# Performance work log

Measured on AMD Instinct MI355X. Metric: run time of the kernel, lower is better.

## Reference

```python
import jax, jax.numpy as jnp
import numpy as np

LEAK_RATE = 0.2
SPECTRAL_RADIUS = 0.9


def setup_inputs() -> dict:
    key = jax.random.key(0)
    k1, k2, k3 = jax.random.split(key, 3)
    B, T, D, U = 32, 1024, 256, 1024
    # glorot-uniform-like init
    lim_w = np.sqrt(6.0 / (U + U)).astype(np.float32)
    lim_in = np.sqrt(6.0 / (D + U)).astype(np.float32)
    W = jax.random.uniform(k1, (U, U), jnp.float32, -lim_w, lim_w)
    # rescale reservoir to target spectral radius (done once at build, like the tf layer)
    eig = np.linalg.eigvals(np.asarray(W))
    W = W * (SPECTRAL_RADIUS / np.max(np.abs(eig)).astype(np.float32))
    W_in = jax.random.uniform(k2, (D, U), jnp.float32, -lim_in, lim_in)
    x = jax.random.normal(k3, (B, T, D), jnp.float32)
    return {"x": x, "W": W, "W_in": W_in}


def reference(x, W, W_in):
    # x: [B, T, D] -> outputs [B, T, U]
    B = x.shape[0]
    U = W.shape[0]
    # precompute input projection for all timesteps: [B, T, U]
    xin = jnp.einsum('btd,du->btu', x, W_in)
    xin_t = jnp.swapaxes(xin, 0, 1)  # [T, B, U]

    def step(h, u_t):
        h_new = (1.0 - LEAK_RATE) * h + LEAK_RATE * jnp.tanh(u_t + h @ W)
        return h_new, h_new

    h0 = jnp.zeros((B, U), x.dtype)
    _, ys = jax.lax.scan(step, h0, xin_t)  # ys: [T, B, U]
    return jnp.swapaxes(ys, 0, 1)  # [B, T, U]
```

## Files before the change

### kernel.cpp

```cpp
#include <hip/hip_runtime.h>
#include <stdint.h>


#define T_   1024
#define D_   256
#define U_   1024
#define NTHR 512
#define HLS  1296
#define BAIL 65536u

typedef _Float16     f16x8 __attribute__((ext_vector_type(8)));
typedef float        f32x4 __attribute__((ext_vector_type(4)));
typedef unsigned int u32x4 __attribute__((ext_vector_type(4)));

#if defined(__has_builtin) && __has_builtin(__builtin_amdgcn_rcpf)
__device__ __forceinline__ float rcp_fast(float v) { return __builtin_amdgcn_rcpf(v); }
#else
__device__ __forceinline__ float rcp_fast(float v) { return 1.f / v; }
#endif

__device__ __forceinline__ float tanh_fast(float v) {
    float e = __expf(2.f * v);
    return 1.f - 2.f * rcp_fast(e + 1.f);
}

__global__ __launch_bounds__(NTHR, 2) void k_recur(const float* __restrict__ x,
                                                   const float* __restrict__ W,
                                                   const float* __restrict__ win,
                                                   float* __restrict__ out,
                                                   u32x4* __restrict__ hc) {
    __shared__ short hl16[4 * HLS];
    __shared__ f32x4 part4[256];
    unsigned int* hl32 = (unsigned int*)hl16;

    const int tid  = threadIdx.x;
    const int dom  = blockIdx.x & 7;
    const int wg   = blockIdx.x >> 3;
    const int c0   = wg * 32;
    const int b0   = dom * 4;
    const int lane = tid & 63;
    const int wv   = tid >> 6;
    const int l15  = lane & 15;
    const int lg   = lane >> 4;

    f16x8 bw[5][2];
#pragma unroll
    for (int kt = 0; kt < 4; ++kt)
#pragma unroll
        for (int ct = 0; ct < 2; ++ct)
#pragma unroll
            for (int j = 0; j < 8; ++j)
                bw[kt][ct][j] =
                    (_Float16)W[(size_t)(wv * 128 + kt * 32 + lg * 8 + j) * U_ + c0 + ct * 16 + l15];
#pragma unroll
    for (int ct = 0; ct < 2; ++ct)
#pragma unroll
        for (int j = 0; j < 8; ++j)
            bw[4][ct][j] =
                (_Float16)win[(size_t)(wv * 32 + lg * 8 + j) * U_ + c0 + ct * 16 + l15];

    for (int i = tid; i < 2 * HLS; i += NTHR) hl32[i] = 0;

    const int xb = tid >> 7, xk = tid & 127;
    float2 pre = *(const float2*)&x[((size_t)(b0 + xb) * T_) * D_ + xk * 2];

    const int abase = (l15 & 3) * HLS + lg * 8;

    float hs0 = 0.f, hs1 = 0.f, hs2 = 0.f, hs3 = 0.f;

    for (int t = 0; t < T_; ++t) {
        __syncthreads();

        {
            unsigned a = (unsigned)__builtin_bit_cast(unsigned short, (_Float16)pre.x);
            unsigned b = (unsigned)__builtin_bit_cast(unsigned short, (_Float16)pre.y);
            hl32[xb * (HLS / 2) + 512 + xk] = a | (b << 16);
        }
        if (t + 1 < T_)
            pre = *(const float2*)&x[((size_t)(b0 + xb) * T_ + (t + 1)) * D_ + xk * 2];

        if (t > 0) {
            const u32x4* pp = hc + (size_t)((t & 1) * 8192 + dom * 1024 + 2 * tid);
            u32x4 va, vb;
            unsigned spin = 0;
            int ok;
            do {
                asm volatile(
                    "global_load_dwordx4 %0, %2, off sc0 sc1\n\t"
                    "global_load_dwordx4 %1, %2, off offset:16 sc0 sc1\n\t"
                    "s_waitcnt vmcnt(0)"
                    : "=&v"(va), "=&v"(vb) : "v"(pp) : "memory");
                unsigned tg = (unsigned)t;
                ok = ((va[0] & 0xffffu) == tg) & ((va[1] & 0xffffu) == tg) &
                     ((va[2] & 0xffffu) == tg) & ((va[3] & 0xffffu) == tg) &
                     ((vb[0] & 0xffffu) == tg) & ((vb[1] & 0xffffu) == tg) &
                     ((vb[2] & 0xffffu) == tg) & ((vb[3] & 0xffffu) == tg);
            } while (!__all(ok) && ++spin < BAIL);
#pragma unroll
            for (int b = 0; b < 4; ++b)
                hl32[b * (HLS / 2) + tid] = (va[b] >> 16) | (vb[b] & 0xffff0000u);
        }
        __syncthreads();

        f32x4 acc0 = {0.f, 0.f, 0.f, 0.f}, acc1 = {0.f, 0.f, 0.f, 0.f};
#pragma unroll
        for (int kt = 0; kt < 5; ++kt) {
            int k0 = (kt < 4) ? (wv * 128 + kt * 32) : (1024 + wv * 32);
            f16x8 av = *reinterpret_cast<const f16x8*>(&hl16[abase + k0]);
            acc0 = __builtin_amdgcn_mfma_f32_16x16x32_f16(av, bw[kt][0], acc0, 0, 0, 0);
            acc1 = __builtin_amdgcn_mfma_f32_16x16x32_f16(av, bw[kt][1], acc1, 0, 0, 0);
        }
        if (lane < 16) {
            part4[wv * 32 + l15]      = acc0;
            part4[wv * 32 + 16 + l15] = acc1;
        }
        __syncthreads();

        if (tid < 32) {
            f32x4 s = part4[tid];
#pragma unroll
            for (int w2 = 1; w2 < 8; ++w2) s += part4[w2 * 32 + tid];
            float h0 = 0.8f * hs0 + 0.2f * tanh_fast(s[0]);
            float h1 = 0.8f * hs1 + 0.2f * tanh_fast(s[1]);
            float h2 = 0.8f * hs2 + 0.2f * tanh_fast(s[2]);
            float h3 = 0.8f * hs3 + 0.2f * tanh_fast(s[3]);
            hs0 = h0; hs1 = h1; hs2 = h2; hs3 = h3;
            size_t ob = ((size_t)b0 * T_ + t) * U_ + c0 + tid;
            out[ob]                       = h0;
            out[ob + (size_t)T_ * U_]     = h1;
            out[ob + (size_t)2 * T_ * U_] = h2;
            out[ob + (size_t)3 * T_ * U_] = h3;
            unsigned tg = (unsigned)(t + 1) & 0xffffu;
            u32x4 pk;
            pk[0] = ((unsigned)__builtin_bit_cast(unsigned short, (_Float16)h0) << 16) | tg;
            pk[1] = ((unsigned)__builtin_bit_cast(unsigned short, (_Float16)h1) << 16) | tg;
            pk[2] = ((unsigned)__builtin_bit_cast(unsigned short, (_Float16)h2) << 16) | tg;
            pk[3] = ((unsigned)__builtin_bit_cast(unsigned short, (_Float16)h3) << 16) | tg;
            u32x4* dst = hc + (size_t)((((t + 1) & 1) * 8192) + dom * 1024 + c0 + tid);
            asm volatile("global_store_dwordx4 %0, %1, off sc0 sc1"
                         :: "v"(dst), "v"(pk) : "memory");
        }
    }
}

extern "C" void kernel_launch(void* const* d_in, const int* in_sizes, int n_in,
                              void* d_out, int out_size, void* d_ws, size_t ws_size,
                              hipStream_t stream) {
    const float* x   = (const float*)d_in[0];
    const float* W   = (const float*)d_in[1];
    const float* win = (const float*)d_in[2];
    float* out = (float*)d_out;

    u32x4* hc = (u32x4*)d_ws;
    if (ws_size < 2 * 8 * 1024 * 16) return;

    k_recur<<<dim3(256), dim3(NTHR), 0, stream>>>(x, W, win, out, hc);
}
```

Baseline: 1.516 ms.

## Load x directly into MFMA registers and publish h before output stores

```diff
diff --git a/kernel.cpp b/kernel.cpp
--- a/kernel.cpp
+++ b/kernel.cpp
@@ -6,8 +6,8 @@
 #define D_   256
 #define U_   1024
 #define NTHR 512
-#define HLS  1296
-#define BAIL 65536u
+#define HROW 1040
+#define BAIL (1u << 20)
 
 typedef _Float16     f16x8 __attribute__((ext_vector_type(8)));
 typedef float        f32x4 __attribute__((ext_vector_type(4)));
@@ -24,12 +24,16 @@
     return 1.f - 2.f * rcp_fast(e + 1.f);
 }
 
+__device__ __forceinline__ unsigned f2u16(_Float16 v) {
+    return (unsigned)__builtin_bit_cast(unsigned short, v);
+}
+
 __global__ __launch_bounds__(NTHR, 2) void k_recur(const float* __restrict__ x,
                                                    const float* __restrict__ W,
                                                    const float* __restrict__ win,
                                                    float* __restrict__ out,
                                                    u32x4* __restrict__ hc) {
-    __shared__ short hl16[4 * HLS];
+    __shared__ short hl16[4 * HROW];
     __shared__ f32x4 part4[256];
     unsigned int* hl32 = (unsigned int*)hl16;
 
@@ -59,29 +63,22 @@
             bw[4][ct][j] =
                 (_Float16)win[(size_t)(wv * 32 + lg * 8 + j) * U_ + c0 + ct * 16 + l15];
 
-    for (int i = tid; i < 2 * HLS; i += NTHR) hl32[i] = 0;
+    for (int i = tid; i < 2 * HROW; i += NTHR) hl32[i] = 0;
+    __syncthreads();
 
-    const int xb = tid >> 7, xk = tid & 127;
-    float2 pre = *(const float2*)&x[((size_t)(b0 + xb) * T_) * D_ + xk * 2];
-
-    const int abase = (l15 & 3) * HLS + lg * 8;
+    const int ab = (l15 & 3) * HROW + lg * 8;
+    const float* xg = &x[((size_t)(b0 + (l15 & 3)) * T_) * D_ + wv * 32 + lg * 8];
 
     float hs0 = 0.f, hs1 = 0.f, hs2 = 0.f, hs3 = 0.f;
 
     for (int t = 0; t < T_; ++t) {
-        __syncthreads();
+        float4 xa = *(const float4*)xg;
+        float4 xc = *(const float4*)(xg + 4);
+        xg += D_;
 
-        {
-            unsigned a = (unsigned)__builtin_bit_cast(unsigned short, (_Float16)pre.x);
-            unsigned b = (unsigned)__builtin_bit_cast(unsigned short, (_Float16)pre.y);
-            hl32[xb * (HLS / 2) + 512 + xk] = a | (b << 16);
-        }
-        if (t + 1 < T_)
-            pre = *(const float2*)&x[((size_t)(b0 + xb) * T_ + (t + 1)) * D_ + xk * 2];
-
+        u32x4 va, vb;
         if (t > 0) {
             const u32x4* pp = hc + (size_t)((t & 1) * 8192 + dom * 1024 + 2 * tid);
-            u32x4 va, vb;
             unsigned spin = 0;
             int ok;
             do {
@@ -89,7 +86,8 @@
                     "global_load_dwordx4 %0, %2, off sc0 sc1\n\t"
                     "global_load_dwordx4 %1, %2, off offset:16 sc0 sc1\n\t"
                     "s_waitcnt vmcnt(0)"
-                    : "=&v"(va), "=&v"(vb) : "v"(pp) : "memory");
+                    : "=&v"(va), "=&v"(vb)
+                    : "v"(pp) : "memory");
                 unsigned tg = (unsigned)t;
                 ok = ((va[0] & 0xffffu) == tg) & ((va[1] & 0xffffu) == tg) &
                      ((va[2] & 0xffffu) == tg) & ((va[3] & 0xffffu) == tg) &
@@ -98,18 +96,27 @@
             } while (!__all(ok) && ++spin < BAIL);
 #pragma unroll
             for (int b = 0; b < 4; ++b)
-                hl32[b * (HLS / 2) + tid] = (va[b] >> 16) | (vb[b] & 0xffff0000u);
+                hl32[b * (HROW / 2) + tid] = (va[b] >> 16) | (vb[b] & 0xffff0000u);
         }
+
+        f16x8 xf;
+        xf[0] = (_Float16)xa.x; xf[1] = (_Float16)xa.y;
+        xf[2] = (_Float16)xa.z; xf[3] = (_Float16)xa.w;
+        xf[4] = (_Float16)xc.x; xf[5] = (_Float16)xc.y;
+        xf[6] = (_Float16)xc.z; xf[7] = (_Float16)xc.w;
+
         __syncthreads();
 
         f32x4 acc0 = {0.f, 0.f, 0.f, 0.f}, acc1 = {0.f, 0.f, 0.f, 0.f};
 #pragma unroll
-        for (int kt = 0; kt < 5; ++kt) {
-            int k0 = (kt < 4) ? (wv * 128 + kt * 32) : (1024 + wv * 32);
-            f16x8 av = *reinterpret_cast<const f16x8*>(&hl16[abase + k0]);
+        for (int kt = 0; kt < 4; ++kt) {
+            f16x8 av = *reinterpret_cast<const f16x8*>(&hl16[ab + wv * 128 + kt * 32]);
             acc0 = __builtin_amdgcn_mfma_f32_16x16x32_f16(av, bw[kt][0], acc0, 0, 0, 0);
             acc1 = __builtin_amdgcn_mfma_f32_16x16x32_f16(av, bw[kt][1], acc1, 0, 0, 0);
         }
+        acc0 = __builtin_amdgcn_mfma_f32_16x16x32_f16(xf, bw[4][0], acc0, 0, 0, 0);
+        acc1 = __builtin_amdgcn_mfma_f32_16x16x32_f16(xf, bw[4][1], acc1, 0, 0, 0);
+
         if (lane < 16) {
             part4[wv * 32 + l15]      = acc0;
             part4[wv * 32 + 16 + l15] = acc1;
@@ -125,21 +132,24 @@
             float h2 = 0.8f * hs2 + 0.2f * tanh_fast(s[2]);
             float h3 = 0.8f * hs3 + 0.2f * tanh_fast(s[3]);
             hs0 = h0; hs1 = h1; hs2 = h2; hs3 = h3;
+            unsigned tg = (unsigned)(t + 1) & 0xffffu;
+            unsigned p0 = (f2u16((_Float16)h0) << 16) | tg;
+            unsigned p1 = (f2u16((_Float16)h1) << 16) | tg;
+            unsigned p2 = (f2u16((_Float16)h2) << 16) | tg;
+            unsigned p3 = (f2u16((_Float16)h3) << 16) | tg;
+            unsigned long long q0 = (unsigned long long)p0 | ((unsigned long long)p1 << 32);
+            unsigned long long q1 = (unsigned long long)p2 | ((unsigned long long)p3 << 32);
+            unsigned long long* dst = (unsigned long long*)
+                (hc + (size_t)((((t + 1) & 1) * 8192) + dom * 1024 + c0 + tid));
+            __hip_atomic_store(&dst[0], q0, __ATOMIC_RELAXED, __HIP_MEMORY_SCOPE_AGENT);
+            __hip_atomic_store(&dst[1], q1, __ATOMIC_RELAXED, __HIP_MEMORY_SCOPE_AGENT);
             size_t ob = ((size_t)b0 * T_ + t) * U_ + c0 + tid;
             out[ob]                       = h0;
             out[ob + (size_t)T_ * U_]     = h1;
             out[ob + (size_t)2 * T_ * U_] = h2;
             out[ob + (size_t)3 * T_ * U_] = h3;
-            unsigned tg = (unsigned)(t + 1) & 0xffffu;
-            u32x4 pk;
-            pk[0] = ((unsigned)__builtin_bit_cast(unsigned short, (_Float16)h0) << 16) | tg;
-            pk[1] = ((unsigned)__builtin_bit_cast(unsigned short, (_Float16)h1) << 16) | tg;
-            pk[2] = ((unsigned)__builtin_bit_cast(unsigned short, (_Float16)h2) << 16) | tg;
-            pk[3] = ((unsigned)__builtin_bit_cast(unsigned short, (_Float16)h3) << 16) | tg;
-            u32x4* dst = hc + (size_t)((((t + 1) & 1) * 8192) + dom * 1024 + c0 + tid);
-            asm volatile("global_store_dwordx4 %0, %1, off sc0 sc1"
-                         :: "v"(dst), "v"(pk) : "memory");
         }
+        __syncthreads();
     }
 }
 
@@ -154,5 +164,6 @@
     u32x4* hc = (u32x4*)d_ws;
     if (ws_size < 2 * 8 * 1024 * 16) return;
 
+    hipMemsetAsync(d_ws, 0, 2 * 8 * 1024 * 16, stream);
     k_recur<<<dim3(256), dim3(NTHR), 0, stream>>>(x, W, win, out, hc);
 }
```

Result: slower. 1.843 ms (+21.6%).
